# Optimization experiments

Measured on AMD Instinct MI355X. Metric: run time of the kernel, lower is better.

## Reference

```python
import jax, jax.numpy as jnp
import numpy as np

NUM_EXPERTS = 8
TOP_K = 2
HIDDEN = 2048
INTER = 1408
TOKENS = 4096


def setup_inputs() -> dict:
    key = jax.random.key(0)
    ks = jax.random.split(key, 5)
    scale_h = 1.0 / np.sqrt(HIDDEN)
    scale_i = 1.0 / np.sqrt(INTER)
    return {
        "x": jax.random.normal(ks[0], (TOKENS, HIDDEN), dtype=jnp.float32),
        "router_w": jax.random.normal(ks[1], (NUM_EXPERTS, HIDDEN), dtype=jnp.float32) * scale_h,
        "w_gate": jax.random.normal(ks[2], (NUM_EXPERTS, HIDDEN, INTER), dtype=jnp.float32) * scale_h,
        "w_up": jax.random.normal(ks[3], (NUM_EXPERTS, HIDDEN, INTER), dtype=jnp.float32) * scale_h,
        "w_down": jax.random.normal(ks[4], (NUM_EXPERTS, INTER, HIDDEN), dtype=jnp.float32) * scale_i,
    }


def reference(x, router_w, w_gate, w_up, w_down):
    # Router: softmax over experts, top-k, renormalize top-k probs
    logits = x @ router_w.T                       # [T, E]
    probs = jax.nn.softmax(logits, axis=-1)
    top_vals, top_idx = jax.lax.top_k(probs, TOP_K)  # [T, K]
    top_vals = top_vals / jnp.sum(top_vals, axis=-1, keepdims=True)
    # Combine weights: [T, E], zero for unselected experts
    t_ar = jnp.arange(x.shape[0])[:, None]
    combine = jnp.zeros((x.shape[0], NUM_EXPERTS), dtype=x.dtype).at[t_ar, top_idx].add(top_vals)
    # Expert SwiGLU FFN: down( silu(x@gate) * (x@up) ), weighted combine.
    # Loop over the small fixed expert set (8); each iteration is a dense GEMM chain.
    out = jnp.zeros_like(x)
    for e in range(NUM_EXPERTS):
        h = jax.nn.silu(x @ w_gate[e]) * (x @ w_up[e])  # [T, INTER]
        out = out + combine[:, e:e + 1] * (h @ w_down[e])
    return out
```

## Files before the change

kernel.cpp:

```cpp
#include <hip/hip_runtime.h>
#include <hip/hip_bf16.h>
#include <cstdint>
#include <cstddef>

#define TOKENS 4096
#define HIDDEN 2048
#define INTER  1408
#define NE     8
#define NGU    2816
#define CAP_ROWS 9216

typedef __bf16 bf16;
typedef __bf16 bf16x8 __attribute__((ext_vector_type(8)));
typedef float  f32x4  __attribute__((ext_vector_type(4)));

__device__ __forceinline__ void async16(const void* g, void* l) {
  __builtin_amdgcn_global_load_lds((const __attribute__((address_space(1))) void*)g,
                                   (__attribute__((address_space(3))) void*)l,
                                   16, 0, 0);
}

__global__ void router_kernel(const float* __restrict__ x, const float* __restrict__ rw,
                              bf16* __restrict__ xb, int* __restrict__ cnt,
                              int* __restrict__ tok, float* __restrict__ wts) {
  const int w = threadIdx.x >> 6, l = threadIdx.x & 63;
  const int t = blockIdx.x * 4 + w;
  const float4* x4 = (const float4*)(x + (size_t)t * HIDDEN);
  const float4* r4 = (const float4*)rw;
  float acc[NE];
#pragma unroll
  for (int e = 0; e < NE; ++e) acc[e] = 0.f;
#pragma unroll
  for (int c = 0; c < 8; ++c) {
    const int idx = c * 64 + l;
    const float4 v = x4[idx];
    bf16* dst = xb + (size_t)t * HIDDEN + idx * 4;
    dst[0] = (bf16)v.x; dst[1] = (bf16)v.y; dst[2] = (bf16)v.z; dst[3] = (bf16)v.w;
#pragma unroll
    for (int e = 0; e < NE; ++e) {
      const float4 u = r4[e * 512 + idx];
      acc[e] += v.x * u.x + v.y * u.y + v.z * u.z + v.w * u.w;
    }
  }
#pragma unroll
  for (int e = 0; e < NE; ++e)
#pragma unroll
    for (int s = 32; s > 0; s >>= 1) acc[e] += __shfl_xor(acc[e], s, 64);
  if (l == 0) {
    int i0 = 0; float l0 = acc[0];
#pragma unroll
    for (int e = 1; e < NE; ++e) if (acc[e] > l0) { l0 = acc[e]; i0 = e; }
    int i1 = -1; float l1 = -3.4e38f;
#pragma unroll
    for (int e = 0; e < NE; ++e) if (e != i0 && acc[e] > l1) { l1 = acc[e]; i1 = e; }
    const float w0 = 1.f / (1.f + __expf(l1 - l0));
    const float w1 = 1.f - w0;
    int p = atomicAdd(&cnt[i0], 1); tok[i0 * 4096 + p] = t; wts[i0 * 4096 + p] = w0;
    p = atomicAdd(&cnt[i1], 1);     tok[i1 * 4096 + p] = t; wts[i1 * 4096 + p] = w1;
  }
}

__global__ void scan_kernel(const int* __restrict__ cnt, int* __restrict__ offs) {
  if (threadIdx.x == 0 && blockIdx.x == 0) {
    int o = 0;
    for (int e = 0; e < NE; ++e) { offs[e] = o; o += ((cnt[e] + 127) >> 7) << 7; }
    offs[NE] = o;
  }
}

__global__ __launch_bounds__(256) void transpose64(
    const float* __restrict__ in, bf16* __restrict__ out, int R, int C,
    size_t inSlab, size_t outSlab, int mode) {
  __shared__ float tile[64][68];
  in  += blockIdx.z * inSlab;
  out += blockIdx.z * outSlab;
  const int c0 = blockIdx.x * 64, r0 = blockIdx.y * 64;
  const int t = threadIdx.x;
  const int row = t >> 4, cq = t & 15;
  const float* src = in + (size_t)(r0 + row) * C + c0 + cq * 4;
#pragma unroll
  for (int p = 0; p < 4; ++p) {
    const float4 v = *(const float4*)(src + (size_t)(p * 16) * C);
    *(float4*)&tile[p * 16 + row][cq * 4] = v;
  }
  __syncthreads();
  const int oc = t >> 2, rq = t & 3;
  float vals[16];
#pragma unroll
  for (int i = 0; i < 16; ++i) vals[i] = tile[rq * 16 + i][oc];
  const int c = c0 + oc;
  int p;
  if (mode == 0) p = c;
  else p = ((c >> 4) << 5) + (c & 15) + (mode == 2 ? 16 : 0);
  bf16x8 o0, o1;
#pragma unroll
  for (int i = 0; i < 8; ++i) { o0[i] = (bf16)vals[i]; o1[i] = (bf16)vals[8 + i]; }
  bf16* dst = out + (size_t)p * R + r0 + rq * 16;
  *(bf16x8*)dst = o0;
  *(bf16x8*)(dst + 8) = o1;
}

__global__ __launch_bounds__(256, 4) void gemm_gateup(
    const bf16* __restrict__ X, const bf16* __restrict__ W, bf16* __restrict__ H,
    const int* __restrict__ cnt, const int* __restrict__ offs,
    const int* __restrict__ tok, const float* __restrict__ wts) {
  const int bid = blockIdx.x;
  const int e = bid & 7;
  const int s = bid >> 3;
  const int mt = s & 31;
  const int nt = s >> 5;
  const int c = cnt[e];
  if (mt * 128 >= c) return;

  __shared__ bf16 sA[128 * 32];
  __shared__ bf16 sB[128 * 32];

  const int t = threadIdx.x, l = t & 63, w = t >> 6;
  const int iA0 = t, iA1 = t + 256;
  const int rA0 = iA0 >> 2, g0 = iA0 & 3;
  const int rA1 = iA1 >> 2, g1 = iA1 & 3;
  const int gr0 = tok[e * 4096 + (mt * 128 + rA0 < c ? mt * 128 + rA0 : c - 1)];
  const int gr1 = tok[e * 4096 + (mt * 128 + rA1 < c ? mt * 128 + rA1 : c - 1)];
  const bf16* pa0 = X + (size_t)gr0 * HIDDEN + g0 * 8;
  const bf16* pa1 = X + (size_t)gr1 * HIDDEN + g1 * 8;
  const bf16* pb0 = W + ((size_t)e * NGU + nt * 128 + rA0) * HIDDEN + g0 * 8;
  const bf16* pb1 = W + ((size_t)e * NGU + nt * 128 + rA1) * HIDDEN + g1 * 8;
  bf16* la0 = sA + iA0 * 8; bf16* la1 = sA + iA1 * 8;
  bf16* lb0 = sB + iA0 * 8; bf16* lb1 = sB + iA1 * 8;

  const int wm = (w >> 1) * 64, wn = (w & 1) * 64;
  const int r16 = l & 15, quad = l >> 4;
  const bf16* fA = sA + (wm + r16) * 32 + quad * 8;
  const bf16* fB = sB + (wn + r16) * 32 + quad * 8;

  f32x4 acc[4][4];
#pragma unroll
  for (int i = 0; i < 4; ++i)
#pragma unroll
    for (int j = 0; j < 4; ++j) acc[i][j] = (f32x4){0.f, 0.f, 0.f, 0.f};

  for (int kk = 0; kk < HIDDEN; kk += 32) {
    async16(pa0 + kk, la0); async16(pa1 + kk, la1);
    async16(pb0 + kk, lb0); async16(pb1 + kk, lb1);
    __syncthreads();
    bf16x8 a[4], b[4];
#pragma unroll
    for (int i = 0; i < 4; ++i) a[i] = *(const bf16x8*)(fA + i * 16 * 32);
#pragma unroll
    for (int j = 0; j < 4; ++j) b[j] = *(const bf16x8*)(fB + j * 16 * 32);
#pragma unroll
    for (int i = 0; i < 4; ++i)
#pragma unroll
      for (int j = 0; j < 4; ++j)
        acc[i][j] = __builtin_amdgcn_mfma_f32_16x16x32_bf16(a[i], b[j], acc[i][j], 0, 0, 0);
    __syncthreads();
  }

  const int mLoc = mt * 128 + wm + quad * 4;
  const int hcol = nt * 64 + (wn >> 1) + r16;
#pragma unroll
  for (int i = 0; i < 4; ++i)
#pragma unroll
    for (int r = 0; r < 4; ++r) {
      const int m = mLoc + i * 16 + r;
      const int mc = m < c ? m : c - 1;
      const float ws = wts[e * 4096 + mc];
      const float g0v = acc[i][0][r], u0v = acc[i][1][r];
      const float g1v = acc[i][2][r], u1v = acc[i][3][r];
      const float h0 = (g0v / (1.f + __expf(-g0v))) * u0v * ws;
      const float h1 = (g1v / (1.f + __expf(-g1v))) * u1v * ws;
      bf16* dst = H + (size_t)(offs[e] + m) * INTER + hcol;
      dst[0]  = (bf16)h0;
      dst[16] = (bf16)h1;
    }
}

__global__ __launch_bounds__(256, 4) void gemm_down(
    const bf16* __restrict__ Hin, const bf16* __restrict__ W, float* __restrict__ out,
    const int* __restrict__ cnt, const int* __restrict__ offs,
    const int* __restrict__ tok) {
  const int bid = blockIdx.x;
  const int e = bid & 7;
  const int s = bid >> 3;
  const int mt = s & 31;
  const int nt = s >> 5;
  const int c = cnt[e];
  if (mt * 128 >= c) return;

  __shared__ bf16 sA[128 * 32];
  __shared__ bf16 sB[128 * 32];

  const int t = threadIdx.x, l = t & 63, w = t >> 6;
  const int iA0 = t, iA1 = t + 256;
  const int rA0 = iA0 >> 2, g0 = iA0 & 3;
  const int rA1 = iA1 >> 2, g1 = iA1 & 3;
  const int base = offs[e] + mt * 128;
  const bf16* pa0 = Hin + (size_t)(base + rA0) * INTER + g0 * 8;
  const bf16* pa1 = Hin + (size_t)(base + rA1) * INTER + g1 * 8;
  const bf16* pb0 = W + ((size_t)e * HIDDEN + nt * 128 + rA0) * INTER + g0 * 8;
  const bf16* pb1 = W + ((size_t)e * HIDDEN + nt * 128 + rA1) * INTER + g1 * 8;
  bf16* la0 = sA + iA0 * 8; bf16* la1 = sA + iA1 * 8;
  bf16* lb0 = sB + iA0 * 8; bf16* lb1 = sB + iA1 * 8;

  const int wm = (w >> 1) * 64, wn = (w & 1) * 64;
  const int r16 = l & 15, quad = l >> 4;
  const bf16* fA = sA + (wm + r16) * 32 + quad * 8;
  const bf16* fB = sB + (wn + r16) * 32 + quad * 8;

  f32x4 acc[4][4];
#pragma unroll
  for (int i = 0; i < 4; ++i)
#pragma unroll
    for (int j = 0; j < 4; ++j) acc[i][j] = (f32x4){0.f, 0.f, 0.f, 0.f};

  for (int kk = 0; kk < INTER; kk += 32) {
    async16(pa0 + kk, la0); async16(pa1 + kk, la1);
    async16(pb0 + kk, lb0); async16(pb1 + kk, lb1);
    __syncthreads();
    bf16x8 a[4], b[4];
#pragma unroll
    for (int i = 0; i < 4; ++i) a[i] = *(const bf16x8*)(fA + i * 16 * 32);
#pragma unroll
    for (int j = 0; j < 4; ++j) b[j] = *(const bf16x8*)(fB + j * 16 * 32);
#pragma unroll
    for (int i = 0; i < 4; ++i)
#pragma unroll
      for (int j = 0; j < 4; ++j)
        acc[i][j] = __builtin_amdgcn_mfma_f32_16x16x32_bf16(a[i], b[j], acc[i][j], 0, 0, 0);
    __syncthreads();
  }

  const int mBase = mt * 128 + wm + quad * 4;
  const int colBase = nt * 128 + wn + r16;
#pragma unroll
  for (int i = 0; i < 4; ++i)
#pragma unroll
    for (int r = 0; r < 4; ++r) {
      const int m = mBase + i * 16 + r;
      if (m < c) {
        const int tkn = tok[e * 4096 + m];
        float* dst = out + (size_t)tkn * HIDDEN + colBase;
#pragma unroll
        for (int j = 0; j < 4; ++j) atomicAdd(dst + j * 16, acc[i][j][r]);
      }
    }
}

extern "C" void kernel_launch(void* const* d_in, const int* in_sizes, int n_in,
                              void* d_out, int out_size, void* d_ws, size_t ws_size,
                              hipStream_t stream) {
  const float* x  = (const float*)d_in[0];
  const float* rw = (const float*)d_in[1];
  const float* wg = (const float*)d_in[2];
  const float* wu = (const float*)d_in[3];
  const float* wd = (const float*)d_in[4];
  float* out = (float*)d_out;

  char* ws = (char*)d_ws;
  size_t o = 0;
  auto alloc = [&](size_t b) { void* p = ws + o; o += (b + 255) & ~(size_t)255; return p; };
  int*   cnt  = (int*)alloc(NE * 4);
  int*   offs = (int*)alloc((NE + 1) * 4);
  int*   tok  = (int*)alloc((size_t)NE * 4096 * 4);
  float* wts  = (float*)alloc((size_t)NE * 4096 * 4);
  bf16*  xb   = (bf16*)alloc((size_t)TOKENS * HIDDEN * 2);
  bf16*  wgu  = (bf16*)alloc((size_t)NE * NGU * HIDDEN * 2);
  bf16*  wdt  = (bf16*)alloc((size_t)NE * HIDDEN * INTER * 2);
  bf16*  h    = (bf16*)alloc((size_t)CAP_ROWS * INTER * 2);

  hipMemsetAsync(cnt, 0, NE * 4, stream);
  hipMemsetAsync(d_out, 0, (size_t)TOKENS * HIDDEN * 4, stream);

  router_kernel<<<TOKENS / 4, 256, 0, stream>>>(x, rw, xb, cnt, tok, wts);
  scan_kernel<<<1, 64, 0, stream>>>(cnt, offs);

  transpose64<<<dim3(INTER / 64, HIDDEN / 64, NE), 256, 0, stream>>>(
      wg, wgu, HIDDEN, INTER, (size_t)HIDDEN * INTER, (size_t)NGU * HIDDEN, 1);
  transpose64<<<dim3(INTER / 64, HIDDEN / 64, NE), 256, 0, stream>>>(
      wu, wgu, HIDDEN, INTER, (size_t)HIDDEN * INTER, (size_t)NGU * HIDDEN, 2);
  transpose64<<<dim3(HIDDEN / 64, INTER / 64, NE), 256, 0, stream>>>(
      wd, wdt, INTER, HIDDEN, (size_t)INTER * HIDDEN, (size_t)HIDDEN * INTER, 0);

  gemm_gateup<<<dim3(NE * (TOKENS / 128) * (NGU / 128)), 256, 0, stream>>>(
      xb, wgu, h, cnt, offs, tok, wts);
  gemm_down<<<dim3(NE * (TOKENS / 128) * (HIDDEN / 128)), 256, 0, stream>>>(
      h, wdt, out, cnt, offs, tok);
}
```

Baseline: 694.5 us.

## Double-buffer GEMM LDS tiles and replace atomic scatter with gather combine

Both expert GEMMs now use two LDS buffers, so the async global-to-LDS load of the next K slice is issued before the MFMAs on the current slice, with one barrier per iteration instead of two. The down projection writes per-slot rows to a scratch buffer (reusing the gate/up weight workspace) instead of doing fp32 atomicAdds into the output. A new combine kernel gathers each token's two expert rows through an inverse index recorded by the router. This drops the output memset and the atomic contention, at the cost of an extra kernel and an extra write and read of the expert outputs.

Measured after the change: 692.7 us. About the same (-0.3%).

```diff
diff --git a/kernel.cpp b/kernel.cpp
--- a/kernel.cpp
+++ b/kernel.cpp
@@ -22,7 +22,8 @@
 
 __global__ void router_kernel(const float* __restrict__ x, const float* __restrict__ rw,
                               bf16* __restrict__ xb, int* __restrict__ cnt,
-                              int* __restrict__ tok, float* __restrict__ wts) {
+                              int* __restrict__ tok, float* __restrict__ wts,
+                              int* __restrict__ inv) {
   const int w = threadIdx.x >> 6, l = threadIdx.x & 63;
   const int t = blockIdx.x * 4 + w;
   const float4* x4 = (const float4*)(x + (size_t)t * HIDDEN);
@@ -55,8 +56,10 @@
     for (int e = 0; e < NE; ++e) if (e != i0 && acc[e] > l1) { l1 = acc[e]; i1 = e; }
     const float w0 = 1.f / (1.f + __expf(l1 - l0));
     const float w1 = 1.f - w0;
-    int p = atomicAdd(&cnt[i0], 1); tok[i0 * 4096 + p] = t; wts[i0 * 4096 + p] = w0;
-    p = atomicAdd(&cnt[i1], 1);     tok[i1 * 4096 + p] = t; wts[i1 * 4096 + p] = w1;
+    int p = atomicAdd(&cnt[i0], 1);
+    tok[i0 * 4096 + p] = t; wts[i0 * 4096 + p] = w0; inv[t * 2]     = (i0 << 12) | p;
+    p = atomicAdd(&cnt[i1], 1);
+    tok[i1 * 4096 + p] = t; wts[i1 * 4096 + p] = w1; inv[t * 2 + 1] = (i1 << 12) | p;
   }
 }
 
@@ -112,8 +115,8 @@
   const int c = cnt[e];
   if (mt * 128 >= c) return;
 
-  __shared__ bf16 sA[128 * 32];
-  __shared__ bf16 sB[128 * 32];
+  __shared__ bf16 sA[2][128 * 32];
+  __shared__ bf16 sB[2][128 * 32];
 
   const int t = threadIdx.x, l = t & 63, w = t >> 6;
   const int iA0 = t, iA1 = t + 256;
@@ -125,13 +128,13 @@
   const bf16* pa1 = X + (size_t)gr1 * HIDDEN + g1 * 8;
   const bf16* pb0 = W + ((size_t)e * NGU + nt * 128 + rA0) * HIDDEN + g0 * 8;
   const bf16* pb1 = W + ((size_t)e * NGU + nt * 128 + rA1) * HIDDEN + g1 * 8;
-  bf16* la0 = sA + iA0 * 8; bf16* la1 = sA + iA1 * 8;
-  bf16* lb0 = sB + iA0 * 8; bf16* lb1 = sB + iA1 * 8;
+  bf16* la0 = sA[0] + iA0 * 8; bf16* la1 = sA[0] + iA1 * 8;
+  bf16* lb0 = sB[0] + iA0 * 8; bf16* lb1 = sB[0] + iA1 * 8;
 
   const int wm = (w >> 1) * 64, wn = (w & 1) * 64;
   const int r16 = l & 15, quad = l >> 4;
-  const bf16* fA = sA + (wm + r16) * 32 + quad * 8;
-  const bf16* fB = sB + (wn + r16) * 32 + quad * 8;
+  const bf16* fA = sA[0] + (wm + r16) * 32 + quad * 8;
+  const bf16* fB = sB[0] + (wn + r16) * 32 + quad * 8;
 
   f32x4 acc[4][4];
 #pragma unroll
@@ -139,21 +142,40 @@
 #pragma unroll
     for (int j = 0; j < 4; ++j) acc[i][j] = (f32x4){0.f, 0.f, 0.f, 0.f};
 
-  for (int kk = 0; kk < HIDDEN; kk += 32) {
-    async16(pa0 + kk, la0); async16(pa1 + kk, la1);
-    async16(pb0 + kk, lb0); async16(pb1 + kk, lb1);
-    __syncthreads();
+  async16(pa0, la0); async16(pa1, la1);
+  async16(pb0, lb0); async16(pb1, lb1);
+  __syncthreads();
+  int cur = 0;
+  for (int kk = 32; kk < HIDDEN; kk += 32) {
+    const int so = (cur ^ 1) * 4096;
+    async16(pa0 + kk, la0 + so); async16(pa1 + kk, la1 + so);
+    async16(pb0 + kk, lb0 + so); async16(pb1 + kk, lb1 + so);
+    const int co = cur * 4096;
     bf16x8 a[4], b[4];
 #pragma unroll
-    for (int i = 0; i < 4; ++i) a[i] = *(const bf16x8*)(fA + i * 16 * 32);
-#pragma unroll
-    for (int j = 0; j < 4; ++j) b[j] = *(const bf16x8*)(fB + j * 16 * 32);
+    for (int i = 0; i < 4; ++i) a[i] = *(const bf16x8*)(fA + co + i * 16 * 32);
+#pragma unroll
+    for (int j = 0; j < 4; ++j) b[j] = *(const bf16x8*)(fB + co + j * 16 * 32);
 #pragma unroll
     for (int i = 0; i < 4; ++i)
 #pragma unroll
       for (int j = 0; j < 4; ++j)
         acc[i][j] = __builtin_amdgcn_mfma_f32_16x16x32_bf16(a[i], b[j], acc[i][j], 0, 0, 0);
     __syncthreads();
+    cur ^= 1;
+  }
+  {
+    const int co = cur * 4096;
+    bf16x8 a[4], b[4];
+#pragma unroll
+    for (int i = 0; i < 4; ++i) a[i] = *(const bf16x8*)(fA + co + i * 16 * 32);
+#pragma unroll
+    for (int j = 0; j < 4; ++j) b[j] = *(const bf16x8*)(fB + co + j * 16 * 32);
+#pragma unroll
+    for (int i = 0; i < 4; ++i)
+#pragma unroll
+      for (int j = 0; j < 4; ++j)
+        acc[i][j] = __builtin_amdgcn_mfma_f32_16x16x32_bf16(a[i], b[j], acc[i][j], 0, 0, 0);
   }
 
   const int mLoc = mt * 128 + wm + quad * 4;
@@ -176,9 +198,8 @@
 }
 
 __global__ __launch_bounds__(256, 4) void gemm_down(
-    const bf16* __restrict__ Hin, const bf16* __restrict__ W, float* __restrict__ out,
-    const int* __restrict__ cnt, const int* __restrict__ offs,
-    const int* __restrict__ tok) {
+    const bf16* __restrict__ Hin, const bf16* __restrict__ W, float* __restrict__ ybuf,
+    const int* __restrict__ cnt, const int* __restrict__ offs) {
   const int bid = blockIdx.x;
   const int e = bid & 7;
   const int s = bid >> 3;
@@ -187,8 +208,8 @@
   const int c = cnt[e];
   if (mt * 128 >= c) return;
 
-  __shared__ bf16 sA[128 * 32];
-  __shared__ bf16 sB[128 * 32];
+  __shared__ bf16 sA[2][128 * 32];
+  __shared__ bf16 sB[2][128 * 32];
 
   const int t = threadIdx.x, l = t & 63, w = t >> 6;
   const int iA0 = t, iA1 = t + 256;
@@ -199,13 +220,13 @@
   const bf16* pa1 = Hin + (size_t)(base + rA1) * INTER + g1 * 8;
   const bf16* pb0 = W + ((size_t)e * HIDDEN + nt * 128 + rA0) * INTER + g0 * 8;
   const bf16* pb1 = W + ((size_t)e * HIDDEN + nt * 128 + rA1) * INTER + g1 * 8;
-  bf16* la0 = sA + iA0 * 8; bf16* la1 = sA + iA1 * 8;
-  bf16* lb0 = sB + iA0 * 8; bf16* lb1 = sB + iA1 * 8;
+  bf16* la0 = sA[0] + iA0 * 8; bf16* la1 = sA[0] + iA1 * 8;
+  bf16* lb0 = sB[0] + iA0 * 8; bf16* lb1 = sB[0] + iA1 * 8;
 
   const int wm = (w >> 1) * 64, wn = (w & 1) * 64;
   const int r16 = l & 15, quad = l >> 4;
-  const bf16* fA = sA + (wm + r16) * 32 + quad * 8;
-  const bf16* fB = sB + (wn + r16) * 32 + quad * 8;
+  const bf16* fA = sA[0] + (wm + r16) * 32 + quad * 8;
+  const bf16* fB = sB[0] + (wn + r16) * 32 + quad * 8;
 
   f32x4 acc[4][4];
 #pragma unroll
@@ -213,21 +234,40 @@
 #pragma unroll
     for (int j = 0; j < 4; ++j) acc[i][j] = (f32x4){0.f, 0.f, 0.f, 0.f};
 
-  for (int kk = 0; kk < INTER; kk += 32) {
-    async16(pa0 + kk, la0); async16(pa1 + kk, la1);
-    async16(pb0 + kk, lb0); async16(pb1 + kk, lb1);
-    __syncthreads();
+  async16(pa0, la0); async16(pa1, la1);
+  async16(pb0, lb0); async16(pb1, lb1);
+  __syncthreads();
+  int cur = 0;
+  for (int kk = 32; kk < INTER; kk += 32) {
+    const int so = (cur ^ 1) * 4096;
+    async16(pa0 + kk, la0 + so); async16(pa1 + kk, la1 + so);
+    async16(pb0 + kk, lb0 + so); async16(pb1 + kk, lb1 + so);
+    const int co = cur * 4096;
     bf16x8 a[4], b[4];
 #pragma unroll
-    for (int i = 0; i < 4; ++i) a[i] = *(const bf16x8*)(fA + i * 16 * 32);
-#pragma unroll
-    for (int j = 0; j < 4; ++j) b[j] = *(const bf16x8*)(fB + j * 16 * 32);
+    for (int i = 0; i < 4; ++i) a[i] = *(const bf16x8*)(fA + co + i * 16 * 32);
+#pragma unroll
+    for (int j = 0; j < 4; ++j) b[j] = *(const bf16x8*)(fB + co + j * 16 * 32);
 #pragma unroll
     for (int i = 0; i < 4; ++i)
 #pragma unroll
       for (int j = 0; j < 4; ++j)
         acc[i][j] = __builtin_amdgcn_mfma_f32_16x16x32_bf16(a[i], b[j], acc[i][j], 0, 0, 0);
     __syncthreads();
+    cur ^= 1;
+  }
+  {
+    const int co = cur * 4096;
+    bf16x8 a[4], b[4];
+#pragma unroll
+    for (int i = 0; i < 4; ++i) a[i] = *(const bf16x8*)(fA + co + i * 16 * 32);
+#pragma unroll
+    for (int j = 0; j < 4; ++j) b[j] = *(const bf16x8*)(fB + co + j * 16 * 32);
+#pragma unroll
+    for (int i = 0; i < 4; ++i)
+#pragma unroll
+      for (int j = 0; j < 4; ++j)
+        acc[i][j] = __builtin_amdgcn_mfma_f32_16x16x32_bf16(a[i], b[j], acc[i][j], 0, 0, 0);
   }
 
   const int mBase = mt * 128 + wm + quad * 4;
@@ -238,12 +278,25 @@
     for (int r = 0; r < 4; ++r) {
       const int m = mBase + i * 16 + r;
       if (m < c) {
-        const int tkn = tok[e * 4096 + m];
-        float* dst = out + (size_t)tkn * HIDDEN + colBase;
-#pragma unroll
-        for (int j = 0; j < 4; ++j) atomicAdd(dst + j * 16, acc[i][j][r]);
+        float* dst = ybuf + (size_t)(offs[e] + m) * HIDDEN + colBase;
+#pragma unroll
+        for (int j = 0; j < 4; ++j) dst[j * 16] = acc[i][j][r];
       }
     }
+}
+
+__global__ __launch_bounds__(256) void combine_kernel(
+    const float* __restrict__ y, const int* __restrict__ inv,
+    const int* __restrict__ offs, float* __restrict__ out) {
+  const int idx = blockIdx.x * 256 + threadIdx.x;
+  const int tkn = idx >> 9, q = idx & 511;
+  const int v0 = inv[tkn * 2], v1 = inv[tkn * 2 + 1];
+  const size_t r0 = (size_t)(offs[v0 >> 12] + (v0 & 4095));
+  const size_t r1 = (size_t)(offs[v1 >> 12] + (v1 & 4095));
+  const float4 a = ((const float4*)y)[r0 * 512 + q];
+  const float4 b = ((const float4*)y)[r1 * 512 + q];
+  float4 o; o.x = a.x + b.x; o.y = a.y + b.y; o.z = a.z + b.z; o.w = a.w + b.w;
+  ((float4*)out)[idx] = o;
 }
 
 extern "C" void kernel_launch(void* const* d_in, const int* in_sizes, int n_in,
@@ -263,15 +316,16 @@
   int*   offs = (int*)alloc((NE + 1) * 4);
   int*   tok  = (int*)alloc((size_t)NE * 4096 * 4);
   float* wts  = (float*)alloc((size_t)NE * 4096 * 4);
+  int*   inv  = (int*)alloc((size_t)TOKENS * 2 * 4);
   bf16*  xb   = (bf16*)alloc((size_t)TOKENS * HIDDEN * 2);
   bf16*  wgu  = (bf16*)alloc((size_t)NE * NGU * HIDDEN * 2);
   bf16*  wdt  = (bf16*)alloc((size_t)NE * HIDDEN * INTER * 2);
   bf16*  h    = (bf16*)alloc((size_t)CAP_ROWS * INTER * 2);
+  float* ybuf = (float*)wgu;
 
   hipMemsetAsync(cnt, 0, NE * 4, stream);
-  hipMemsetAsync(d_out, 0, (size_t)TOKENS * HIDDEN * 4, stream);
-
-  router_kernel<<<TOKENS / 4, 256, 0, stream>>>(x, rw, xb, cnt, tok, wts);
+
+  router_kernel<<<TOKENS / 4, 256, 0, stream>>>(x, rw, xb, cnt, tok, wts, inv);
   scan_kernel<<<1, 64, 0, stream>>>(cnt, offs);
 
   transpose64<<<dim3(INTER / 64, HIDDEN / 64, NE), 256, 0, stream>>>(
@@ -284,5 +338,7 @@
   gemm_gateup<<<dim3(NE * (TOKENS / 128) * (NGU / 128)), 256, 0, stream>>>(
       xb, wgu, h, cnt, offs, tok, wts);
   gemm_down<<<dim3(NE * (TOKENS / 128) * (HIDDEN / 128)), 256, 0, stream>>>(
-      h, wdt, out, cnt, offs, tok);
-}
+      h, wdt, ybuf, cnt, offs);
+  combine_kernel<<<dim3(TOKENS * (HIDDEN / 4) / 256), 256, 0, stream>>>(
+      ybuf, inv, offs, out);
+}
```

## Replace atomic scatter in down GEMM with row-major buffer plus combine kernel

Applied to the files above, without the earlier changes.

The down-projection epilogue now writes each expert's output rows with vectorized stores into a staging buffer (aliased onto the gate/up weight buffer), instead of doing per-element float atomics into the output. A new combine kernel sums each token's two expert rows using an inverse map recorded by the router, and the output memset is dropped. The MFMA operand order is swapped so that each lane holds four consecutive columns, which allows the vector stores in both GEMM epilogues. The three transpose launches are merged into a single prep_weights launch, and the LDS tile padding changes from 68 to 65. This adds one extra pass over the intermediate outputs in exchange for removing atomic contention.

After: 678.5 us. 1.02x faster.

```diff
diff --git a/kernel.cpp b/kernel.cpp
--- a/kernel.cpp
+++ b/kernel.cpp
@@ -12,6 +12,7 @@
 
 typedef __bf16 bf16;
 typedef __bf16 bf16x8 __attribute__((ext_vector_type(8)));
+typedef __bf16 bf16x4 __attribute__((ext_vector_type(4)));
 typedef float  f32x4  __attribute__((ext_vector_type(4)));
 
 __device__ __forceinline__ void async16(const void* g, void* l) {
@@ -22,7 +23,8 @@
 
 __global__ void router_kernel(const float* __restrict__ x, const float* __restrict__ rw,
                               bf16* __restrict__ xb, int* __restrict__ cnt,
-                              int* __restrict__ tok, float* __restrict__ wts) {
+                              int* __restrict__ tok, float* __restrict__ wts,
+                              int* __restrict__ inv) {
   const int w = threadIdx.x >> 6, l = threadIdx.x & 63;
   const int t = blockIdx.x * 4 + w;
   const float4* x4 = (const float4*)(x + (size_t)t * HIDDEN);
@@ -55,8 +57,10 @@
     for (int e = 0; e < NE; ++e) if (e != i0 && acc[e] > l1) { l1 = acc[e]; i1 = e; }
     const float w0 = 1.f / (1.f + __expf(l1 - l0));
     const float w1 = 1.f - w0;
-    int p = atomicAdd(&cnt[i0], 1); tok[i0 * 4096 + p] = t; wts[i0 * 4096 + p] = w0;
-    p = atomicAdd(&cnt[i1], 1);     tok[i1 * 4096 + p] = t; wts[i1 * 4096 + p] = w1;
+    int p = atomicAdd(&cnt[i0], 1);
+    tok[i0 * 4096 + p] = t; wts[i0 * 4096 + p] = w0; inv[t * 2]     = (i0 << 12) | p;
+    p = atomicAdd(&cnt[i1], 1);
+    tok[i1 * 4096 + p] = t; wts[i1 * 4096 + p] = w1; inv[t * 2 + 1] = (i1 << 12) | p;
   }
 }
 
@@ -68,13 +72,23 @@
   }
 }
 
-__global__ __launch_bounds__(256) void transpose64(
-    const float* __restrict__ in, bf16* __restrict__ out, int R, int C,
-    size_t inSlab, size_t outSlab, int mode) {
-  __shared__ float tile[64][68];
-  in  += blockIdx.z * inSlab;
-  out += blockIdx.z * outSlab;
-  const int c0 = blockIdx.x * 64, r0 = blockIdx.y * 64;
+__global__ __launch_bounds__(256) void prep_weights(
+    const float* __restrict__ wg, const float* __restrict__ wu, const float* __restrict__ wd,
+    bf16* __restrict__ wgu, bf16* __restrict__ wdt) {
+  __shared__ float tile[64][65];
+  const int bid = blockIdx.x;
+  const int which = bid / 5632;
+  const int rem = bid - which * 5632;
+  const int e = rem & 7;
+  const int tid2 = rem >> 3;
+  const float* in; bf16* out; int R, C, c0, r0, mode;
+  if (which == 2) {
+    in = wd + (size_t)e * INTER * HIDDEN; out = wdt + (size_t)e * HIDDEN * INTER;
+    R = INTER; C = HIDDEN; c0 = (tid2 & 31) * 64; r0 = (tid2 >> 5) * 64; mode = 0;
+  } else {
+    in = (which ? wu : wg) + (size_t)e * HIDDEN * INTER; out = wgu + (size_t)e * NGU * HIDDEN;
+    R = HIDDEN; C = INTER; c0 = (tid2 % 22) * 64; r0 = (tid2 / 22) * 64; mode = which + 1;
+  }
   const int t = threadIdx.x;
   const int row = t >> 4, cq = t & 15;
   const float* src = in + (size_t)(r0 + row) * C + c0 + cq * 4;
@@ -152,33 +166,35 @@
     for (int i = 0; i < 4; ++i)
 #pragma unroll
       for (int j = 0; j < 4; ++j)
-        acc[i][j] = __builtin_amdgcn_mfma_f32_16x16x32_bf16(a[i], b[j], acc[i][j], 0, 0, 0);
+        acc[i][j] = __builtin_amdgcn_mfma_f32_16x16x32_bf16(b[j], a[i], acc[i][j], 0, 0, 0);
     __syncthreads();
   }
 
-  const int mLoc = mt * 128 + wm + quad * 4;
-  const int hcol = nt * 64 + (wn >> 1) + r16;
-#pragma unroll
-  for (int i = 0; i < 4; ++i)
-#pragma unroll
-    for (int r = 0; r < 4; ++r) {
-      const int m = mLoc + i * 16 + r;
-      const int mc = m < c ? m : c - 1;
-      const float ws = wts[e * 4096 + mc];
-      const float g0v = acc[i][0][r], u0v = acc[i][1][r];
-      const float g1v = acc[i][2][r], u1v = acc[i][3][r];
-      const float h0 = (g0v / (1.f + __expf(-g0v))) * u0v * ws;
-      const float h1 = (g1v / (1.f + __expf(-g1v))) * u1v * ws;
-      bf16* dst = H + (size_t)(offs[e] + m) * INTER + hcol;
-      dst[0]  = (bf16)h0;
-      dst[16] = (bf16)h1;
+  const int mRowBase = mt * 128 + wm + r16;
+  const int hcolBase = nt * 64 + (wn >> 1) + quad * 4;
+#pragma unroll
+  for (int i = 0; i < 4; ++i) {
+    const int m = mRowBase + i * 16;
+    const int mc = m < c ? m : c - 1;
+    const float ws = wts[e * 4096 + mc];
+    bf16* rowp = H + (size_t)(offs[e] + m) * INTER;
+#pragma unroll
+    for (int jp = 0; jp < 2; ++jp) {
+      bf16x4 hv;
+#pragma unroll
+      for (int r = 0; r < 4; ++r) {
+        const float g = acc[i][2 * jp][r];
+        const float u = acc[i][2 * jp + 1][r];
+        hv[r] = (bf16)((g / (1.f + __expf(-g))) * u * ws);
+      }
+      *(bf16x4*)(rowp + hcolBase + jp * 16) = hv;
     }
+  }
 }
 
 __global__ __launch_bounds__(256, 4) void gemm_down(
-    const bf16* __restrict__ Hin, const bf16* __restrict__ W, float* __restrict__ out,
-    const int* __restrict__ cnt, const int* __restrict__ offs,
-    const int* __restrict__ tok) {
+    const bf16* __restrict__ Hin, const bf16* __restrict__ W, float* __restrict__ ybuf,
+    const int* __restrict__ cnt, const int* __restrict__ offs) {
   const int bid = blockIdx.x;
   const int e = bid & 7;
   const int s = bid >> 3;
@@ -226,24 +242,36 @@
     for (int i = 0; i < 4; ++i)
 #pragma unroll
       for (int j = 0; j < 4; ++j)
-        acc[i][j] = __builtin_amdgcn_mfma_f32_16x16x32_bf16(a[i], b[j], acc[i][j], 0, 0, 0);
+        acc[i][j] = __builtin_amdgcn_mfma_f32_16x16x32_bf16(b[j], a[i], acc[i][j], 0, 0, 0);
     __syncthreads();
   }
 
-  const int mBase = mt * 128 + wm + quad * 4;
-  const int colBase = nt * 128 + wn + r16;
-#pragma unroll
-  for (int i = 0; i < 4; ++i)
-#pragma unroll
-    for (int r = 0; r < 4; ++r) {
-      const int m = mBase + i * 16 + r;
-      if (m < c) {
-        const int tkn = tok[e * 4096 + m];
-        float* dst = out + (size_t)tkn * HIDDEN + colBase;
-#pragma unroll
-        for (int j = 0; j < 4; ++j) atomicAdd(dst + j * 16, acc[i][j][r]);
-      }
+  const int mRowBase = mt * 128 + wm + r16;
+  const int colBase = nt * 128 + wn + quad * 4;
+#pragma unroll
+  for (int i = 0; i < 4; ++i) {
+    const int m = mRowBase + i * 16;
+    if (m < c) {
+      float* rowp = ybuf + (size_t)(offs[e] + m) * HIDDEN + colBase;
+#pragma unroll
+      for (int j = 0; j < 4; ++j)
+        *(f32x4*)(rowp + j * 16) = acc[i][j];
     }
+  }
+}
+
+__global__ __launch_bounds__(256) void combine_kernel(
+    const float* __restrict__ y, const int* __restrict__ inv,
+    const int* __restrict__ offs, float* __restrict__ out) {
+  const int idx = blockIdx.x * 256 + threadIdx.x;
+  const int tkn = idx >> 9, q = idx & 511;
+  const int v0 = inv[tkn * 2], v1 = inv[tkn * 2 + 1];
+  const size_t r0 = (size_t)(offs[v0 >> 12] + (v0 & 4095));
+  const size_t r1 = (size_t)(offs[v1 >> 12] + (v1 & 4095));
+  const float4 a = ((const float4*)y)[r0 * 512 + q];
+  const float4 b = ((const float4*)y)[r1 * 512 + q];
+  float4 o; o.x = a.x + b.x; o.y = a.y + b.y; o.z = a.z + b.z; o.w = a.w + b.w;
+  ((float4*)out)[idx] = o;
 }
 
 extern "C" void kernel_launch(void* const* d_in, const int* in_sizes, int n_in,
@@ -263,26 +291,24 @@
   int*   offs = (int*)alloc((NE + 1) * 4);
   int*   tok  = (int*)alloc((size_t)NE * 4096 * 4);
   float* wts  = (float*)alloc((size_t)NE * 4096 * 4);
+  int*   inv  = (int*)alloc((size_t)TOKENS * 2 * 4);
   bf16*  xb   = (bf16*)alloc((size_t)TOKENS * HIDDEN * 2);
   bf16*  wgu  = (bf16*)alloc((size_t)NE * NGU * HIDDEN * 2);
   bf16*  wdt  = (bf16*)alloc((size_t)NE * HIDDEN * INTER * 2);
   bf16*  h    = (bf16*)alloc((size_t)CAP_ROWS * INTER * 2);
+  float* ybuf = (float*)wgu;
 
   hipMemsetAsync(cnt, 0, NE * 4, stream);
-  hipMemsetAsync(d_out, 0, (size_t)TOKENS * HIDDEN * 4, stream);
-
-  router_kernel<<<TOKENS / 4, 256, 0, stream>>>(x, rw, xb, cnt, tok, wts);
+
+  router_kernel<<<TOKENS / 4, 256, 0, stream>>>(x, rw, xb, cnt, tok, wts, inv);
   scan_kernel<<<1, 64, 0, stream>>>(cnt, offs);
 
-  transpose64<<<dim3(INTER / 64, HIDDEN / 64, NE), 256, 0, stream>>>(
-      wg, wgu, HIDDEN, INTER, (size_t)HIDDEN * INTER, (size_t)NGU * HIDDEN, 1);
-  transpose64<<<dim3(INTER / 64, HIDDEN / 64, NE), 256, 0, stream>>>(
-      wu, wgu, HIDDEN, INTER, (size_t)HIDDEN * INTER, (size_t)NGU * HIDDEN, 2);
-  transpose64<<<dim3(HIDDEN / 64, INTER / 64, NE), 256, 0, stream>>>(
-      wd, wdt, INTER, HIDDEN, (size_t)INTER * HIDDEN, (size_t)HIDDEN * INTER, 0);
+  prep_weights<<<dim3(3 * 5632), 256, 0, stream>>>(wg, wu, wd, wgu, wdt);
 
   gemm_gateup<<<dim3(NE * (TOKENS / 128) * (NGU / 128)), 256, 0, stream>>>(
       xb, wgu, h, cnt, offs, tok, wts);
   gemm_down<<<dim3(NE * (TOKENS / 128) * (HIDDEN / 128)), 256, 0, stream>>>(
-      h, wdt, out, cnt, offs, tok);
-}
+      h, wdt, ybuf, cnt, offs);
+  combine_kernel<<<dim3(TOKENS * (HIDDEN / 4) / 256), 256, 0, stream>>>(
+      ybuf, inv, offs, out);
+}
```
